# Kernel optimization log

Measured on AMD Instinct MI355X. Metric: run time of the kernel, lower is better.

The kernel has to match this reference:

```python
import jax, jax.numpy as jnp
import numpy as np

VGG_MEAN = jnp.array([0.485, 0.456, 0.406], jnp.float32).reshape(1, 3, 1, 1)
VGG_STD = jnp.array([0.229, 0.224, 0.225], jnp.float32).reshape(1, 3, 1, 1)
SCALE = 2


def _bicubic_matrix(n_in, n_out, a=-0.75):
    # torch F.interpolate(mode='bicubic', align_corners=True): src = i*(n_in-1)/(n_out-1), cubic a=-0.75
    i = np.arange(n_out)
    src = i * (n_in - 1) / (n_out - 1)
    f = np.floor(src).astype(np.int64)
    t = src - f

    def kern(x):
        x = np.abs(x)
        return np.where(x <= 1.0, (a + 2) * x**3 - (a + 3) * x**2 + 1.0,
                        np.where(x < 2.0, a * x**3 - 5 * a * x**2 + 8 * a * x - 4 * a, 0.0))

    M = np.zeros((n_out, n_in), np.float64)
    for off in (-1, 0, 1, 2):
        idx = np.clip(f + off, 0, n_in - 1)
        np.add.at(M, (i, idx), kern(t - off))
    return jnp.asarray(M, jnp.float32)


def _bicubic_up(x, scale):
    B, C, H, W = x.shape
    Mh = _bicubic_matrix(H, H * scale)
    Mw = _bicubic_matrix(W, W * scale)
    x = jnp.einsum('oh,bchw->bcow', Mh, x)
    return jnp.einsum('pw,bcow->bcop', Mw, x)


def _conv(x, w, b, pad):
    y = jax.lax.conv_general_dilated(x, w, (1, 1), ((pad, pad), (pad, pad)),
                                     dimension_numbers=('NCHW', 'OIHW', 'NCHW'))
    return y + b[None, :, None, None]


def _features(x, w1, b1, w2, b2, w3, b3, wm, bm):
    # VGG19 features[0:7] + BasicBlock(128->16, 1x1, LeakyReLU 0.2)
    x = jax.nn.relu(_conv(x, w1, b1, 1))
    x = jax.nn.relu(_conv(x, w2, b2, 1))
    x = jax.lax.reduce_window(x, -jnp.inf, jax.lax.max, (1, 1, 2, 2), (1, 1, 2, 2), 'VALID')
    x = jax.nn.relu(_conv(x, w3, b3, 1))
    x = jax.nn.leaky_relu(_conv(x, wm, bm, 0), 0.2)
    return x


def _patches(x):
    # im2col like F.unfold: output feature dim ordered (C, kh, kw), same as torch
    p = jax.lax.conv_general_dilated_patches(x, (3, 3), (1, 1), ((1, 1), (1, 1)))
    B, Ck, H, W = p.shape
    return p.reshape(B, Ck, H * W)


def _forward(query, key, w1, b1, w2, b2, w3, b3, wm, bm, flag_8k):
    q = (query - VGG_MEAN) / VGG_STD
    if not flag_8k:
        q = _bicubic_up(q, SCALE)
    q = _features(q, w1, b1, w2, b2, w3, b3, wm, bm)
    B, C, Hq, Wq = q.shape
    qp = _patches(q)                                      # [B, C*9, Lq]
    qp = qp / jnp.maximum(jnp.linalg.norm(qp, axis=1, keepdims=True), 1e-12)

    B2, C2, Hk, Wk = key.shape
    k = key.reshape(B2, C2, Hk // SCALE, SCALE, Wk // SCALE, SCALE).mean((3, 5))  # AvgPool2d(scale)
    k = (k - VGG_MEAN) / VGG_STD
    if not flag_8k:
        k = _bicubic_up(k, SCALE)
    k = _features(k, w1, b1, w2, b2, w3, b3, wm, bm)
    kp = jnp.transpose(_patches(k), (0, 2, 1))            # [B, Lk, C*9]
    kp = kp / jnp.maximum(jnp.linalg.norm(kp, axis=2, keepdims=True), 1e-12)

    y = jnp.einsum('bkc,bcq->bkq', kp, qp)                # [B, Lk, Lq] cosine similarities
    rel = jnp.max(y, axis=1).reshape(B, 1, Hq, Wq)
    idx = jnp.argmax(y, axis=1)
    return rel, idx


def setup_inputs():
    key0 = jax.random.key(0)
    ks = jax.random.split(key0, 6)
    return {
        'query': jax.random.uniform(ks[0], (1, 3, 120, 120), jnp.float32),
        'key': jax.random.uniform(ks[1], (1, 3, 240, 240), jnp.float32),
        'w1': jax.random.normal(ks[2], (64, 3, 3, 3), jnp.float32) * 0.05,
        'b1': jnp.zeros((64,), jnp.float32),
        'w2': jax.random.normal(ks[3], (64, 64, 3, 3), jnp.float32) * 0.05,
        'b2': jnp.zeros((64,), jnp.float32),
        'w3': jax.random.normal(ks[4], (128, 64, 3, 3), jnp.float32) * 0.05,
        'b3': jnp.zeros((128,), jnp.float32),
        'wm': jax.random.normal(ks[5], (16, 128, 1, 1), jnp.float32) * 0.05,
        'bm': jnp.zeros((16,), jnp.float32),
        'flag_8k': 0,
    }


def reference(query, key, w1, b1, w2, b2, w3, b3, wm, bm, flag_8k):
    return _forward(query, key, w1, b1, w2, b2, w3, b3, wm, bm, flag_8k)
```

## Files before the change

### kernel.cpp

```cpp
#include <hip/hip_runtime.h>
#include <math.h>

#define H0 120
#define W0 120
#define H1 240
#define W1 240
#define L  14400
#define FDIM 144
#define CPAD 160
#define LPAD 14464

#define KC     128
#define NCHT   113
#define NCHB   8
#define NGRAN  904
#define NLIST  32
#define MARGIN 6.5e-3f

typedef _Float16 half8 __attribute__((ext_vector_type(8)));
typedef float    f32x4 __attribute__((ext_vector_type(4)));

__device__ __forceinline__ double meanc(int c){ return c==0?0.485:(c==1?0.456:0.406); }
__device__ __forceinline__ double stdc (int c){ return c==0?0.229:(c==1?0.224:0.225); }

__global__ __launch_bounds__(256) void k_cvt_all(const float* __restrict__ w1, const float* __restrict__ b1,
                                                 const float* __restrict__ w2, const float* __restrict__ b2,
                                                 const float* __restrict__ w3, const float* __restrict__ b3,
                                                 const float* __restrict__ wm, const float* __restrict__ bm,
                                                 double* __restrict__ wd){
  int i = blockIdx.x*256 + threadIdx.x;
  if (i >= 114640) return;
  float v;
  if      (i < 1728)   v = w1[i];
  else if (i < 1792)   v = b1[i-1728];
  else if (i < 38656)  v = w2[i-1792];
  else if (i < 38720)  v = b2[i-38656];
  else if (i < 112448) v = w3[i-38720];
  else if (i < 112576) v = b3[i-112448];
  else if (i < 114624) v = wm[i-112576];
  else                 v = bm[i-114624];
  wd[i] = (double)v;
}

__global__ __launch_bounds__(256) void k_prep(const float* __restrict__ query,
                                              const float* __restrict__ key,
                                              float* __restrict__ nq){
  int i = blockIdx.x*256 + threadIdx.x;
  if (i >= 2*3*L) return;
  int b = i/(3*L); int r = i - b*3*L; int c = r / L; int p = r - c*L;
  double v;
  if (b==0){
    v = (double)query[c*L + p];
  } else {
    int y = p / W0, x = p - y*W0;
    const float* kk = key + (size_t)c*(H1*W1);
    int yy = 2*y, xx = 2*x;
    v = 0.25*((double)kk[yy*W1+xx] + (double)kk[yy*W1+xx+1]
            + (double)kk[(yy+1)*W1+xx] + (double)kk[(yy+1)*W1+xx+1]);
  }
  nq[i] = (float)((v - meanc(c)) / stdc(c));
}

__device__ __forceinline__ double cubw(double x){
  x = fabs(x);
  if (x <= 1.0)      return (1.25*x - 2.25)*x*x + 1.0;
  else if (x < 2.0)  return -0.75*(((x - 5.0)*x + 8.0)*x - 4.0);
  return 0.0;
}

__global__ __launch_bounds__(256) void k_bicubic(const float* __restrict__ nq,
                                                 float* __restrict__ up){
  int i = blockIdx.x*256 + threadIdx.x;
  if (i >= 2*3*H1*W1) return;
  int bc = i/(H1*W1); int r = i - bc*H1*W1; int oy = r/W1, ox = r - oy*W1;
  double sy = (double)oy * (double)(H0-1) / (double)(H1-1);
  double sx = (double)ox * (double)(W0-1) / (double)(W1-1);
  int fy = (int)floor(sy); double ty = sy - (double)fy;
  int fx = (int)floor(sx); double tx = sx - (double)fx;
  double wy[4], wx[4]; int iy[4], ix[4];
  #pragma unroll
  for (int o=0;o<4;++o){
    wy[o] = cubw(ty - (double)(o-1));
    wx[o] = cubw(tx - (double)(o-1));
    int yv = fy + o - 1; iy[o] = min(max(yv,0),H0-1);
    int xv = fx + o - 1; ix[o] = min(max(xv,0),W0-1);
  }
  const float* src = nq + (size_t)bc*(H0*W0);
  double acc = 0.0;
  #pragma unroll
  for (int j=0;j<4;++j){
    double colv = 0.0;
    #pragma unroll
    for (int a=0;a<4;++a) colv += wy[a]*(double)src[iy[a]*W0 + ix[j]];
    acc += wx[j]*colv;
  }
  up[i] = (float)acc;
}

template<int CIN, int CIC, int HW>
__global__ __launch_bounds__(256) void k_conv3x3(const float* __restrict__ in,
                                                 const double* __restrict__ w,
                                                 const double* __restrict__ bias,
                                                 float* __restrict__ out, int CO){
  constexpr int T = 30, TI = 32, TP = 36;
  constexpr int NT = HW / T;
  __shared__ float s_in[CIC][TI][TP];
  int tid = threadIdx.x;
  int tile = blockIdx.x; int trow = tile/NT;
  int ty0 = trow*T, tx0 = (tile - trow*NT)*T;
  int ocb = blockIdx.y*8; int b = blockIdx.z;
  const float* inb = in + (size_t)b*CIN*HW*HW;
  bool active = tid < 225;
  int tyy = (tid/15)*2, txx = (tid%15)*2;
  double acc[2][2][8];
  #pragma unroll
  for (int o=0;o<8;++o){
    double bv = bias[ocb+o];
    acc[0][0][o]=bv; acc[0][1][o]=bv; acc[1][0][o]=bv; acc[1][1][o]=bv;
  }
  for (int c0=0; c0<CIN; c0+=CIC){
    __syncthreads();
    for (int f4 = tid; f4 < CIC*256; f4 += 256){
      int ci = f4 >> 8; int rem = f4 & 255;
      int rr = rem >> 3; int c4 = rem & 7;
      int gy = ty0 + rr - 1, gx0 = tx0 + c4*4 - 1;
      float4 v = {0.f,0.f,0.f,0.f};
      if (gy >= 0 && gy < HW){
        const float* rowp = inb + (size_t)(c0+ci)*HW*HW + (size_t)gy*HW;
        float* vp = (float*)&v;
        #pragma unroll
        for (int e=0;e<4;++e){
          int gx = gx0 + e;
          if (gx >= 0 && gx < HW) vp[e] = rowp[gx];
        }
      }
      *(float4*)&s_in[ci][rr][c4*4] = v;
    }
    __syncthreads();
    if (active){
      for (int ci=0; ci<CIC; ++ci){
        double tap[4][4];
        #pragma unroll
        for (int rr=0;rr<4;++rr){
          float2 lo = *(const float2*)&s_in[ci][tyy+rr][txx];
          float2 hi = *(const float2*)&s_in[ci][tyy+rr][txx+2];
          tap[rr][0] = (double)lo.x; tap[rr][1] = (double)lo.y;
          tap[rr][2] = (double)hi.x; tap[rr][3] = (double)hi.y;
        }
        const double* wp = w + ((size_t)ocb*CIN + (c0+ci))*9;
        #pragma unroll
        for (int t=0;t<9;++t){
          const int ky = t/3, kx = t - ky*3;
          #pragma unroll
          for (int o=0;o<8;++o){
            double wv = wp[(size_t)o*CIN*9 + t];
            acc[0][0][o] += tap[ky+0][kx+0]*wv;
            acc[0][1][o] += tap[ky+0][kx+1]*wv;
            acc[1][0][o] += tap[ky+1][kx+0]*wv;
            acc[1][1][o] += tap[ky+1][kx+1]*wv;
          }
        }
      }
    }
  }
  if (active){
    #pragma unroll
    for (int py=0;py<2;++py)
      #pragma unroll
      for (int px=0;px<2;++px){
        int gy = ty0+tyy+py, gx = tx0+txx+px;
        float* op = out + ((size_t)(b*CO+ocb)*HW + gy)*HW + gx;
        #pragma unroll
        for (int o=0;o<8;++o){
          double v = acc[py][px][o];
          op[(size_t)o*HW*HW] = (float)(v>0.0 ? v : 0.0);
        }
      }
  }
}

__global__ __launch_bounds__(256) void k_maxpool(const float* __restrict__ in,
                                                 float* __restrict__ out){
  int i = blockIdx.x*256 + threadIdx.x;
  if (i >= 2*64*L) return;
  int bc = i / L; int p = i - bc*L; int y = p/W0, x = p - y*W0;
  const float* s = in + (size_t)bc*H1*W1;
  int yy = 2*y, xx = 2*x;
  out[i] = fmaxf(fmaxf(s[yy*W1+xx], s[yy*W1+xx+1]),
                 fmaxf(s[(yy+1)*W1+xx], s[(yy+1)*W1+xx+1]));
}

__global__ __launch_bounds__(256) void k_conv1x1(const float* __restrict__ in,
                                                 const double* __restrict__ wm,
                                                 const double* __restrict__ bm,
                                                 float* __restrict__ out){
  int i = blockIdx.x*256 + threadIdx.x;
  if (i >= 2*L) return;
  int b = i/L; int p = i - b*L;
  double a[16];
  #pragma unroll
  for (int o=0;o<16;++o) a[o] = bm[o];
  const float* src = in + (size_t)b*128*L + p;
  for (int ci=0; ci<128; ++ci){
    double v = (double)src[(size_t)ci*L];
    #pragma unroll
    for (int o=0;o<16;++o) a[o] += v * wm[o*128 + ci];
  }
  float* dst = out + (size_t)b*16*L + p;
  #pragma unroll
  for (int o=0;o<16;++o){ double v=a[o]; dst[(size_t)o*L] = (float)(v>0.0 ? v : 0.2*v); }
}

__global__ __launch_bounds__(256) void k_patches(const float* __restrict__ fm,
                                                 _Float16* __restrict__ Tq16,
                                                 _Float16* __restrict__ Tk16,
                                                 float* __restrict__ Tq32,
                                                 float* __restrict__ Tk32){
  int i = blockIdx.x*256 + threadIdx.x;
  if (i >= 2*L + (LPAD - L)) return;
  int b, p, row;
  if (i < 2*L){ b = i / L; p = i - b*L; row = p; }
  else        { b = 1; p = L - 1; row = L + (i - 2*L); }
  int y = p/W0, x = p - y*W0;
  const float* src = fm + (size_t)b*16*L;
  double ss = 0.0;
  for (int c=0;c<16;++c){
    #pragma unroll
    for (int dy=0;dy<3;++dy){
      int gy = y+dy-1;
      #pragma unroll
      for (int dx=0;dx<3;++dx){
        int gx = x+dx-1;
        double v = (gy>=0 && gy<H0 && gx>=0 && gx<W0) ? (double)src[c*L + gy*W0 + gx] : 0.0;
        ss += v*v;
      }
    }
  }
  double rn = 1.0 / fmax(sqrt(ss), 1e-12);
  _Float16* d16 = (b==0 ? Tq16 : Tk16) + (size_t)row*CPAD;
  float*    d32 = (b==0 ? Tq32 : Tk32) + (size_t)row*CPAD;
  for (int c=0;c<16;++c){
    #pragma unroll
    for (int dy=0;dy<3;++dy){
      int gy = y+dy-1;
      #pragma unroll
      for (int dx=0;dx<3;++dx){
        int gx = x+dx-1;
        double v = (gy>=0 && gy<H0 && gx>=0 && gx<W0) ? (double)src[c*L + gy*W0 + gx] : 0.0;
        float f = (float)(v*rn);
        int idx = c*9 + dy*3 + dx;
        d32[idx] = f;
        d16[idx] = (_Float16)f;
      }
    }
  }
  for (int c=FDIM;c<CPAD;++c){ d32[c] = 0.f; d16[c] = (_Float16)0.f; }
}

__global__ __launch_bounds__(256) void k_simh(const _Float16* __restrict__ Tq,
                                              const _Float16* __restrict__ Tk,
                                              _Float16* __restrict__ cmaxh){
  __shared__ __align__(16) _Float16 skT[40*512];
  int tid = threadIdx.x;
  int wid = tid >> 6, lane = tid & 63;
  int wk = wid & 1, wq = wid >> 1;
  int q0 = blockIdx.x * 96;
  int cg = lane >> 4;
  int qb = q0 + wq*48 + (lane & 15);
  half8 fB[3][5];
  #pragma unroll
  for (int bf=0; bf<3; ++bf)
    #pragma unroll
    for (int ks=0; ks<5; ++ks)
      fB[bf][ks] = *(const half8*)(Tq + (size_t)(qb + bf*16)*CPAD + ks*32 + cg*8);
  int ch0 = blockIdx.y * NCHB;
  for (int cc=0; cc<NCHB; ++cc){
    int chunk = ch0 + cc;
    if (chunk >= NCHT) break;
    int kbase = chunk * KC;
    __syncthreads();
    #pragma unroll
    for (int it=0; it<10; ++it){
      int b1 = wid*10 + it;
      int kg = b1 / 5, ks = b1 % 5;
      const _Float16* g = Tk + (size_t)(kbase + kg*16 + (lane&15))*CPAD + ks*32 + cg*8;
      __builtin_amdgcn_global_load_lds((const __attribute__((address_space(1))) void*)g,
                                       (__attribute__((address_space(3))) void*)(skT + b1*512),
                                       16, 0, 0);
    }
    __syncthreads();
    f32x4 acc[4][3];
    #pragma unroll
    for (int kf=0;kf<4;++kf)
      #pragma unroll
      for (int bf=0;bf<3;++bf)
        acc[kf][bf] = (f32x4){0.f,0.f,0.f,0.f};
    #pragma unroll
    for (int ks=0; ks<5; ++ks){
      #pragma unroll
      for (int kf=0; kf<4; ++kf){
        half8 av = *(const half8*)(skT + ((size_t)((wk*4+kf)*5 + ks))*512 + lane*8);
        #pragma unroll
        for (int bf=0; bf<3; ++bf)
          acc[kf][bf] = __builtin_amdgcn_mfma_f32_16x16x32_f16(av, fB[bf][ks], acc[kf][bf], 0, 0, 0);
      }
    }
    #pragma unroll
    for (int kf=0; kf<4; ++kf){
      int gran = chunk*8 + wk*4 + kf;
      #pragma unroll
      for (int bf=0; bf<3; ++bf){
        f32x4 a = acc[kf][bf];
        float m = fmaxf(fmaxf(a.x, a.y), fmaxf(a.z, a.w));
        m = fmaxf(m, __shfl_xor(m, 16));
        m = fmaxf(m, __shfl_xor(m, 32));
        float mb = m * (m >= 0.f ? 1.0009765625f : 0.9990234375f);
        if (lane < 16)
          cmaxh[(size_t)gran*L + q0 + wq*48 + bf*16 + lane] = (_Float16)mb;
      }
    }
  }
}

__global__ __launch_bounds__(256) void k_flag(const _Float16* __restrict__ cmaxh,
                                              unsigned short* __restrict__ list,
                                              int* __restrict__ nf,
                                              float* __restrict__ thrv){
  int q    = blockIdx.x*4 + (threadIdx.x >> 6);
  int lane = threadIdx.x & 63;
  if (q >= L) return;
  float v[15];
  #pragma unroll
  for (int j=0;j<15;++j){
    int g = j*64 + lane;
    v[j] = (g < NGRAN) ? (float)cmaxh[(size_t)g*L + q] : -1e30f;
  }
  float m = -1e30f;
  #pragma unroll
  for (int j=0;j<15;++j) m = fmaxf(m, v[j]);
  #pragma unroll
  for (int d=32; d>=1; d>>=1) m = fmaxf(m, __shfl_xor(m, d));
  float thr = m - MARGIN;
  unsigned short* lst = list + (size_t)q*NLIST;
  int base = 0;
  #pragma unroll
  for (int j=0;j<15;++j){
    bool f = v[j] >= thr;
    unsigned long long mask = __ballot(f);
    if (f){
      int pos = base + __popcll(mask & ((1ull<<lane)-1ull));
      if (pos < NLIST) lst[pos] = (unsigned short)(j*64 + lane);
    }
    base += __popcll(mask);
  }
  if (lane == 0){ nf[q] = base; thrv[q] = thr; }
}

__global__ __launch_bounds__(64) void k_rescore3(const float* __restrict__ Tq32,
                                                 const float* __restrict__ Tk32,
                                                 const unsigned short* __restrict__ list,
                                                 const int* __restrict__ nf,
                                                 const float* __restrict__ thrv,
                                                 const _Float16* __restrict__ cmaxh,
                                                 float* __restrict__ out){
  int q = blockIdx.x, lane = threadIdx.x;
  int slot = lane & 15, quarter = lane >> 4;
  const float* qp = Tq32 + (size_t)q*CPAD + quarter*36;
  double q64[36];
  #pragma unroll
  for (int c=0;c<36;++c) q64[c] = (double)qp[c];
  int n = nf[q];
  float thr = thrv[q];
  double best = -1e300; int bi = 0x7fffffff;

  auto proc = [&](int g){
    int key = g*16 + slot;
    const float* kr = Tk32 + (size_t)key*CPAD + quarter*36;
    double s = 0.0;
    #pragma unroll
    for (int c=0;c<36;++c) s += q64[c]*(double)kr[c];
    s += __shfl_xor(s, 16);
    s += __shfl_xor(s, 32);
    if (key < L && s > best){ best = s; bi = key; }
  };

  if (n <= NLIST){
    const unsigned short* lst = list + (size_t)q*NLIST;
    for (int it=0; it<n; ++it) proc(lst[it]);
  } else {
    for (int g=0; g<NGRAN; ++g)
      if ((float)cmaxh[(size_t)g*L + q] >= thr) proc(g);
  }
  #pragma unroll
  for (int d=1; d<16; d<<=1){
    double v2 = __shfl_xor(best, d);
    int    i2 = __shfl_xor(bi, d);
    if (v2 > best || (v2 == best && i2 < bi)){ best = v2; bi = i2; }
  }
  if (lane == 0){
    out[q]     = (float)best;
    out[L + q] = (float)bi;
  }
}

extern "C" void kernel_launch(void* const* d_in, const int* in_sizes, int n_in,
                              void* d_out, int out_size, void* d_ws, size_t ws_size,
                              hipStream_t stream){
  const float* query = (const float*)d_in[0];
  const float* key   = (const float*)d_in[1];
  const float* w1 = (const float*)d_in[2];
  const float* b1 = (const float*)d_in[3];
  const float* w2 = (const float*)d_in[4];
  const float* b2 = (const float*)d_in[5];
  const float* w3 = (const float*)d_in[6];
  const float* b3 = (const float*)d_in[7];
  const float* wm = (const float*)d_in[8];
  const float* bm = (const float*)d_in[9];
  float* out = (float*)d_out;

  double* wd = (double*)d_ws;
  double* wd1 = wd;
  double* bd1 = wd + 1728;
  double* wd2 = wd + 1792;
  double* bd2 = wd + 38656;
  double* wd3 = wd + 38720;
  double* bd3 = wd + 112448;
  double* wdm = wd + 112576;
  double* bdm = wd + 114624;
  float* fbase = (float*)d_ws + 230400;
  float* nq = fbase;
  float* up = nq + 86400;
  float* A  = up + 345600;
  float* Bf = A  + 7372800;
  float* C  = A;
  float* D  = A + 1843200;
  float* FM = Bf + 7372800 - 460800;
  _Float16* Tq16 = (_Float16*)A;
  _Float16* Tk16 = (_Float16*)(A + 1152000);
  float*    Tq32 = A + 2309120;
  float*    Tk32 = Tq32 + 2304000;
  _Float16* cmaxh = (_Float16*)(A + 6927360);
  unsigned short* list = (unsigned short*)(A + 13436160);
  int*   nfl  = (int*)(A + 13666560);
  float* thrv = A + 13680960;

  k_cvt_all<<<(114640+255)/256, 256, 0, stream>>>(w1,b1,w2,b2,w3,b3,wm,bm, wd);

  k_prep   <<<(2*3*L + 255)/256, 256, 0, stream>>>(query, key, nq);
  k_bicubic<<<(2*3*H1*W1 + 255)/256, 256, 0, stream>>>(nq, up);
  k_conv3x3<3,3,240><<<dim3(64,8,2), 256, 0, stream>>>(up, wd1, bd1, A, 64);
  k_conv3x3<64,8,240><<<dim3(64,8,2), 256, 0, stream>>>(A, wd2, bd2, Bf, 64);
  k_maxpool<<<(2*64*L + 255)/256, 256, 0, stream>>>(Bf, C);
  k_conv3x3<64,8,120><<<dim3(16,16,2), 256, 0, stream>>>(C, wd3, bd3, D, 128);
  k_conv1x1<<<(2*L + 255)/256, 256, 0, stream>>>(D, wdm, bdm, FM);
  k_patches<<<(2*L + (LPAD-L) + 255)/256, 256, 0, stream>>>(FM, Tq16, Tk16, Tq32, Tk32);
  k_simh   <<<dim3(150, 15), 256, 0, stream>>>(Tq16, Tk16, cmaxh);
  k_flag   <<<(L + 3)/4, 256, 0, stream>>>(cmaxh, list, nfl, thrv);
  k_rescore3<<<L, 64, 0, stream>>>(Tq32, Tk32, list, nfl, thrv, cmaxh, out);
}
```

Before: 695.6 us.

## Double-buffer conv3x3 shared input tiles with register prefetch and rolling rows

The 3x3 convolution now prefetches the next channel chunk from global memory into registers while computing on the current shared-memory buffer, then writes it into a second buffer, so one barrier per chunk replaces two and global load latency is hidden behind FP64 math. Interior tiles use a vectorized float4 load path without bounds checks, and the tap rows are rolled so only two rows are held as doubles at a time, cutting register use. The channel chunk shrinks from 8 to 4 and launch bounds request 4 blocks per SM for occupancy, at the cost of more chunk iterations and barriers.

```diff
diff --git a/kernel.cpp b/kernel.cpp
--- a/kernel.cpp
+++ b/kernel.cpp
@@ -98,13 +98,14 @@
 }
 
 template<int CIN, int CIC, int HW>
-__global__ __launch_bounds__(256) void k_conv3x3(const float* __restrict__ in,
-                                                 const double* __restrict__ w,
-                                                 const double* __restrict__ bias,
-                                                 float* __restrict__ out, int CO){
+__global__ __launch_bounds__(256, 4) void k_conv3x3(const float* __restrict__ in,
+                                                    const double* __restrict__ w,
+                                                    const double* __restrict__ bias,
+                                                    float* __restrict__ out, int CO){
   constexpr int T = 30, TI = 32, TP = 36;
   constexpr int NT = HW / T;
-  __shared__ float s_in[CIC][TI][TP];
+  constexpr int NCH = CIN / CIC;
+  __shared__ __align__(16) float s_in[2][CIC][TI][TP];
   int tid = threadIdx.x;
   int tile = blockIdx.x; int trow = tile/NT;
   int ty0 = trow*T, tx0 = (tile - trow*NT)*T;
@@ -112,57 +113,94 @@
   const float* inb = in + (size_t)b*CIN*HW*HW;
   bool active = tid < 225;
   int tyy = (tid/15)*2, txx = (tid%15)*2;
+  int srr = tid >> 3, sc4 = tid & 7;
+  int sgy = ty0 + srr - 1, sgx0 = tx0 + sc4*4 - 1;
+  bool interior = (ty0 > 0) && (ty0 + TI - 1 <= HW) && (tx0 > 0) && (tx0 + TI - 1 <= HW);
+
   double acc[2][2][8];
   #pragma unroll
   for (int o=0;o<8;++o){
     double bv = bias[ocb+o];
     acc[0][0][o]=bv; acc[0][1][o]=bv; acc[1][0][o]=bv; acc[1][1][o]=bv;
   }
-  for (int c0=0; c0<CIN; c0+=CIC){
-    __syncthreads();
-    for (int f4 = tid; f4 < CIC*256; f4 += 256){
-      int ci = f4 >> 8; int rem = f4 & 255;
-      int rr = rem >> 3; int c4 = rem & 7;
-      int gy = ty0 + rr - 1, gx0 = tx0 + c4*4 - 1;
-      float4 v = {0.f,0.f,0.f,0.f};
-      if (gy >= 0 && gy < HW){
-        const float* rowp = inb + (size_t)(c0+ci)*HW*HW + (size_t)gy*HW;
-        float* vp = (float*)&v;
-        #pragma unroll
-        for (int e=0;e<4;++e){
-          int gx = gx0 + e;
-          if (gx >= 0 && gx < HW) vp[e] = rowp[gx];
-        }
-      }
-      *(float4*)&s_in[ci][rr][c4*4] = v;
-    }
-    __syncthreads();
-    if (active){
-      for (int ci=0; ci<CIC; ++ci){
-        double tap[4][4];
-        #pragma unroll
-        for (int rr=0;rr<4;++rr){
-          float2 lo = *(const float2*)&s_in[ci][tyy+rr][txx];
-          float2 hi = *(const float2*)&s_in[ci][tyy+rr][txx+2];
-          tap[rr][0] = (double)lo.x; tap[rr][1] = (double)lo.y;
-          tap[rr][2] = (double)hi.x; tap[rr][3] = (double)hi.y;
-        }
-        const double* wp = w + ((size_t)ocb*CIN + (c0+ci))*9;
-        #pragma unroll
-        for (int t=0;t<9;++t){
-          const int ky = t/3, kx = t - ky*3;
+
+  float4 regs[CIC];
+  auto gload = [&](int c0){
+    if (interior){
+      #pragma unroll
+      for (int j=0;j<CIC;++j)
+        regs[j] = *(const float4*)(inb + (size_t)(c0+j)*HW*HW + (size_t)sgy*HW + sgx0);
+    } else {
+      #pragma unroll
+      for (int j=0;j<CIC;++j){
+        float4 v = {0.f,0.f,0.f,0.f};
+        if (sgy >= 0 && sgy < HW){
+          const float* rowp = inb + (size_t)(c0+j)*HW*HW + (size_t)sgy*HW;
+          float* vp = (float*)&v;
           #pragma unroll
-          for (int o=0;o<8;++o){
-            double wv = wp[(size_t)o*CIN*9 + t];
-            acc[0][0][o] += tap[ky+0][kx+0]*wv;
-            acc[0][1][o] += tap[ky+0][kx+1]*wv;
-            acc[1][0][o] += tap[ky+1][kx+0]*wv;
-            acc[1][1][o] += tap[ky+1][kx+1]*wv;
+          for (int e=0;e<4;++e){
+            int gx = sgx0 + e;
+            if (gx >= 0 && gx < HW) vp[e] = rowp[gx];
           }
         }
-      }
-    }
-  }
+        regs[j] = v;
+      }
+    }
+  };
+  auto swrite = [&](int buf){
+    #pragma unroll
+    for (int j=0;j<CIC;++j)
+      *(float4*)&s_in[buf][j][srr][sc4*4] = regs[j];
+  };
+
+  gload(0);
+  swrite(0);
+  __syncthreads();
+  for (int k=0; k<NCH; ++k){
+    int cur = k & 1;
+    if (k+1 < NCH) gload((k+1)*CIC);
+    if (active){
+      #pragma unroll
+      for (int ci=0; ci<CIC; ++ci){
+        const double* wp = w + ((size_t)ocb*CIN + (k*CIC+ci))*9;
+        double r0[4], r1[4];
+        {
+          float2 lo = *(const float2*)&s_in[cur][ci][tyy+0][txx];
+          float2 hi = *(const float2*)&s_in[cur][ci][tyy+0][txx+2];
+          r0[0]=(double)lo.x; r0[1]=(double)lo.y; r0[2]=(double)hi.x; r0[3]=(double)hi.y;
+          lo = *(const float2*)&s_in[cur][ci][tyy+1][txx];
+          hi = *(const float2*)&s_in[cur][ci][tyy+1][txx+2];
+          r1[0]=(double)lo.x; r1[1]=(double)lo.y; r1[2]=(double)hi.x; r1[3]=(double)hi.y;
+        }
+        #pragma unroll
+        for (int ky=0; ky<3; ++ky){
+          #pragma unroll
+          for (int kx=0; kx<3; ++kx){
+            #pragma unroll
+            for (int o=0;o<8;++o){
+              double wv = wp[(size_t)o*CIN*9 + ky*3 + kx];
+              acc[0][0][o] += r0[kx+0]*wv;
+              acc[0][1][o] += r0[kx+1]*wv;
+              acc[1][0][o] += r1[kx+0]*wv;
+              acc[1][1][o] += r1[kx+1]*wv;
+            }
+          }
+          if (ky < 2){
+            #pragma unroll
+            for (int e=0;e<4;++e) r0[e] = r1[e];
+            float2 lo = *(const float2*)&s_in[cur][ci][tyy+ky+2][txx];
+            float2 hi = *(const float2*)&s_in[cur][ci][tyy+ky+2][txx+2];
+            r1[0]=(double)lo.x; r1[1]=(double)lo.y; r1[2]=(double)hi.x; r1[3]=(double)hi.y;
+          }
+        }
+      }
+    }
+    if (k+1 < NCH){
+      swrite(cur ^ 1);
+      __syncthreads();
+    }
+  }
+
   if (active){
     #pragma unroll
     for (int py=0;py<2;++py)
@@ -449,9 +487,9 @@
   k_prep   <<<(2*3*L + 255)/256, 256, 0, stream>>>(query, key, nq);
   k_bicubic<<<(2*3*H1*W1 + 255)/256, 256, 0, stream>>>(nq, up);
   k_conv3x3<3,3,240><<<dim3(64,8,2), 256, 0, stream>>>(up, wd1, bd1, A, 64);
-  k_conv3x3<64,8,240><<<dim3(64,8,2), 256, 0, stream>>>(A, wd2, bd2, Bf, 64);
+  k_conv3x3<64,4,240><<<dim3(64,8,2), 256, 0, stream>>>(A, wd2, bd2, Bf, 64);
   k_maxpool<<<(2*64*L + 255)/256, 256, 0, stream>>>(Bf, C);
-  k_conv3x3<64,8,120><<<dim3(16,16,2), 256, 0, stream>>>(C, wd3, bd3, D, 128);
+  k_conv3x3<64,4,120><<<dim3(16,16,2), 256, 0, stream>>>(C, wd3, bd3, D, 128);
   k_conv1x1<<<(2*L + 255)/256, 256, 0, stream>>>(D, wdm, bdm, FM);
   k_patches<<<(2*L + (LPAD-L) + 255)/256, 256, 0, stream>>>(FM, Tq16, Tk16, Tq32, Tk32);
   k_simh   <<<dim3(150, 15), 256, 0, stream>>>(Tq16, Tk16, cmaxh);
```

Result: slower. 942.6 us (+35.5%).
